# Kernel optimization log

Hardware: AMD Instinct MI355X
Metric: run time of the kernel (lower is better)

## Reference

```python
import jax, jax.numpy as jnp
import numpy as np

B, N, D_IN = 32, 4096, 768
D_SLOT, K = 256, 8
D_SHAPE, D_TEX = 128, 128
NUM_ITERS = 3
EPS = 1e-8
LN_EPS = 1e-5


def _ln(x, g, b):
    m = jnp.mean(x, axis=-1, keepdims=True)
    v = jnp.mean((x - m) ** 2, axis=-1, keepdims=True)
    return (x - m) * jax.lax.rsqrt(v + LN_EPS) * g + b


def setup_inputs() -> dict:
    key = jax.random.key(0)
    ks = jax.random.split(key, 20)
    s = lambda fan_in: 1.0 / np.sqrt(fan_in)
    d = {}
    d['features'] = jax.random.normal(ks[0], (B, N, D_IN), dtype=jnp.float32)
    # slot init MLP: d_input -> 2*d_slot -> K*d_slot
    d['Wi1'] = jax.random.uniform(ks[1], (D_IN, 2 * D_SLOT), minval=-s(D_IN), maxval=s(D_IN))
    d['bi1'] = jnp.zeros((2 * D_SLOT,), jnp.float32)
    d['Wi2'] = jax.random.uniform(ks[2], (2 * D_SLOT, K * D_SLOT), minval=-s(2 * D_SLOT), maxval=s(2 * D_SLOT))
    d['bi2'] = jnp.zeros((K * D_SLOT,), jnp.float32)
    # input_proj Linear + LayerNorm
    d['Wp'] = jax.random.uniform(ks[3], (D_IN, D_SLOT), minval=-s(D_IN), maxval=s(D_IN))
    d['bp'] = jnp.zeros((D_SLOT,), jnp.float32)
    d['ln_in_g'] = jnp.ones((D_SLOT,), jnp.float32)
    d['ln_in_b'] = jnp.zeros((D_SLOT,), jnp.float32)
    # attention projections (no bias)
    d['Wqs'] = jax.random.uniform(ks[4], (D_SHAPE, D_SHAPE), minval=-s(D_SHAPE), maxval=s(D_SHAPE))
    d['Wks'] = jax.random.uniform(ks[5], (D_SHAPE, D_SHAPE), minval=-s(D_SHAPE), maxval=s(D_SHAPE))
    d['Wqt'] = jax.random.uniform(ks[6], (D_TEX, D_TEX), minval=-s(D_TEX), maxval=s(D_TEX))
    d['Wkt'] = jax.random.uniform(ks[7], (D_TEX, D_TEX), minval=-s(D_TEX), maxval=s(D_TEX))
    # GRUCell (PyTorch layout, gate order r,z,n), stored as [in, 3*hidden]
    d['W_ih'] = jax.random.uniform(ks[8], (D_SLOT, 3 * D_SLOT), minval=-s(D_SLOT), maxval=s(D_SLOT))
    d['W_hh'] = jax.random.uniform(ks[9], (D_SLOT, 3 * D_SLOT), minval=-s(D_SLOT), maxval=s(D_SLOT))
    d['b_ih'] = jax.random.uniform(ks[10], (3 * D_SLOT,), minval=-s(D_SLOT), maxval=s(D_SLOT))
    d['b_hh'] = jax.random.uniform(ks[11], (3 * D_SLOT,), minval=-s(D_SLOT), maxval=s(D_SLOT))
    # slot LayerNorm + MLP
    d['ln_g'] = jnp.ones((D_SLOT,), jnp.float32)
    d['ln_b'] = jnp.zeros((D_SLOT,), jnp.float32)
    d['Wm1'] = jax.random.uniform(ks[12], (D_SLOT, 2 * D_SLOT), minval=-s(D_SLOT), maxval=s(D_SLOT))
    d['bm1'] = jnp.zeros((2 * D_SLOT,), jnp.float32)
    d['Wm2'] = jax.random.uniform(ks[13], (2 * D_SLOT, D_SLOT), minval=-s(2 * D_SLOT), maxval=s(2 * D_SLOT))
    d['bm2'] = jnp.zeros((D_SLOT,), jnp.float32)
    return d


def _gru(x, h, W_ih, W_hh, b_ih, b_hh):
    gx = x @ W_ih + b_ih  # [M, 3H]
    gh = h @ W_hh + b_hh
    xr, xz, xn = jnp.split(gx, 3, axis=-1)
    hr, hz, hn = jnp.split(gh, 3, axis=-1)
    r = jax.nn.sigmoid(xr + hr)
    z = jax.nn.sigmoid(xz + hz)
    n = jnp.tanh(xn + r * hn)
    return (1.0 - z) * n + z * h


def reference(features, Wi1, bi1, Wi2, bi2, Wp, bp, ln_in_g, ln_in_b,
              Wqs, Wks, Wqt, Wkt, W_ih, W_hh, b_ih, b_hh,
              ln_g, ln_b, Wm1, bm1, Wm2, bm2):
    gelu = lambda x: jax.nn.gelu(x, approximate=False)
    Bsz = features.shape[0]
    # input projection + LN: [B, N, D_SLOT]
    inputs = _ln(features @ Wp + bp, ln_in_g, ln_in_b)
    # probabilistic slot init (eval mode: deterministic branch only)
    feat_pool = jnp.mean(features, axis=1)  # [B, D_IN]
    slots = (gelu(feat_pool @ Wi1 + bi1) @ Wi2 + bi2).reshape(Bsz, K, D_SLOT)
    inp_s = inputs[:, :, :D_SHAPE]
    inp_t = inputs[:, :, D_SHAPE:]
    k_s = inp_s @ Wks  # [B, N, Ds]
    k_t = inp_t @ Wkt
    scale_s = D_SHAPE ** -0.5
    scale_t = D_TEX ** -0.5
    attn = None
    for _ in range(NUM_ITERS):
        q_s = slots[:, :, :D_SHAPE] @ Wqs  # [B, K, Ds]
        q_t = slots[:, :, D_SHAPE:] @ Wqt
        attn_shape = jnp.einsum('bkd,bnd->bkn', q_s, k_s) * scale_s
        attn_tex = jnp.einsum('bkd,bnd->bkn', q_t, k_t) * scale_t
        logits = 0.7 * attn_shape + 0.3 * attn_tex  # [B, K, N]
        attn = jax.nn.softmax(logits, axis=1)  # softmax over slots
        attn_normed = attn / (jnp.sum(attn, axis=-1, keepdims=True) + EPS)
        updates = jnp.einsum('bkn,bnd->bkd', attn_normed, inputs)
        h = _gru(updates.reshape(Bsz * K, D_SLOT), slots.reshape(Bsz * K, D_SLOT),
                 W_ih, W_hh, b_ih, b_hh).reshape(Bsz, K, D_SLOT)
        sn = _ln(h, ln_g, ln_b)
        slots = h + (gelu(sn @ Wm1 + bm1) @ Wm2 + bm2)
    return slots, attn, slots[:, :, :D_SHAPE], slots[:, :, D_SHAPE:]
```

## Files before the change

kernel.cpp:

```cpp
#include <hip/hip_runtime.h>
#include <math.h>

#define NB 32
#define NN 4096
#define DIN 768
#define DS 256
#define KS 8
#define MROWS (NB*NN)

typedef short s8v __attribute__((ext_vector_type(8)));
typedef float f4v __attribute__((ext_vector_type(4)));

__device__ __forceinline__ short f2bf(float f) {
    unsigned u = __builtin_bit_cast(unsigned, f);
    u = (u + 0x7FFFu + ((u >> 16) & 1u)) >> 16;
    return (short)u;
}
__device__ __forceinline__ float bf2f(short s) {
    unsigned u = ((unsigned)(unsigned short)s) << 16;
    return __builtin_bit_cast(float, u);
}
__device__ __forceinline__ float gelu_exact(float x) {
    return 0.5f * x * (1.0f + erff(x * 0.70710678118654752f));
}

__global__ __launch_bounds__(256) void prep_weights(const float* Wp, const float* Wks,
                                                    const float* Wkt, short* Wp_sw, short* Wk_sw) {
    int t = blockIdx.x * 256 + threadIdx.x;
    if (t < 24 * 16 * 64) {
        int s = t / (16 * 64), nt = (t / 64) % 16, l = t % 64;
        int q = l >> 4, m = l & 15;
        #pragma unroll
        for (int j = 0; j < 8; ++j)
            Wp_sw[t * 8 + j] = f2bf(Wp[(s * 32 + q * 8 + j) * 256 + nt * 16 + m]);
    } else if (t < 24 * 16 * 64 + 2 * 4 * 8 * 64) {
        int t2 = t - 24 * 16 * 64;
        int half = t2 / (4 * 8 * 64);
        int r = t2 % (4 * 8 * 64);
        int s = r / (8 * 64), nt = (r / 64) % 8, l = r % 64;
        int q = l >> 4, m = l & 15;
        const float* W = half ? Wkt : Wks;
        #pragma unroll
        for (int j = 0; j < 8; ++j)
            Wk_sw[t2 * 8 + j] = f2bf(W[(s * 32 + q * 8 + j) * 128 + nt * 16 + m]);
    }
}

__global__ __launch_bounds__(256, 2) void gemm_in_ln(const float* feat, const short* Wp_sw,
                                                     const float* bp, const float* g,
                                                     const float* bb, short* inputs_bf,
                                                     float* ppart) {
    __shared__ short Als[128 * 40];
    __shared__ short Bls[16 * 64 * 8];
    __shared__ float pool_ls[4][768];
    int tid = threadIdx.x;
    int wave = tid >> 6, lane = tid & 63, q = lane >> 4, m = lane & 15;
    long rowblk = (long)blockIdx.x * 128;
    f4v acc[2][16];
    #pragma unroll
    for (int rg = 0; rg < 2; ++rg)
        #pragma unroll
        for (int i = 0; i < 16; ++i) acc[rg][i] = (f4v){0, 0, 0, 0};
    for (int i = tid; i < 4 * 768; i += 256) (&pool_ls[0][0])[i] = 0.0f;
    __syncthreads();
    for (int s = 0; s < 24; ++s) {
        float4 v[4];
        #pragma unroll
        for (int p = 0; p < 4; ++p) {
            int idx = p * 256 + tid;
            int r = idx >> 3, cj = (idx & 7) * 4;
            v[p] = *(const float4*)(feat + (rowblk + r) * 768 + s * 32 + cj);
            short4 pk = make_short4(f2bf(v[p].x), f2bf(v[p].y), f2bf(v[p].z), f2bf(v[p].w));
            *(short4*)&Als[r * 40 + cj] = pk;
        }
        #pragma unroll
        for (int i = 0; i < 4; ++i) {
            int wb = i * 256 + wave * 64;
            __builtin_amdgcn_global_load_lds(
                (const __attribute__((address_space(1))) void*)(Wp_sw + (size_t)s * 8192 +
                                                               (size_t)(wb + lane) * 8),
                (__attribute__((address_space(3))) void*)&Bls[wb * 8], 16, 0, 0);
        }
        __syncthreads();
        {
            float px = v[0].x + v[1].x + v[2].x + v[3].x;
            float py = v[0].y + v[1].y + v[2].y + v[3].y;
            float pz = v[0].z + v[1].z + v[2].z + v[3].z;
            float pw = v[0].w + v[1].w + v[2].w + v[3].w;
            #pragma unroll
            for (int off = 8; off <= 32; off <<= 1) {
                px += __shfl_xor(px, off, 64);
                py += __shfl_xor(py, off, 64);
                pz += __shfl_xor(pz, off, 64);
                pw += __shfl_xor(pw, off, 64);
            }
            if (lane < 8) {
                int col = s * 32 + lane * 4;
                pool_ls[wave][col] += px;
                pool_ls[wave][col + 1] += py;
                pool_ls[wave][col + 2] += pz;
                pool_ls[wave][col + 3] += pw;
            }
        }
        s8v a0 = *(const s8v*)&Als[(wave * 32 + m) * 40 + q * 8];
        s8v a1 = *(const s8v*)&Als[(wave * 32 + 16 + m) * 40 + q * 8];
        #pragma unroll
        for (int nt = 0; nt < 16; ++nt) {
            s8v bf = *(const s8v*)&Bls[(nt * 64 + lane) * 8];
            acc[0][nt] = __builtin_amdgcn_mfma_f32_16x16x32_bf16(a0, bf, acc[0][nt], 0, 0, 0);
            acc[1][nt] = __builtin_amdgcn_mfma_f32_16x16x32_bf16(a1, bf, acc[1][nt], 0, 0, 0);
        }
        __syncthreads();
    }
    #pragma unroll
    for (int rg = 0; rg < 2; ++rg) {
        #pragma unroll
        for (int nt = 0; nt < 16; ++nt) {
            float bpv = bp[nt * 16 + m];
            #pragma unroll
            for (int r = 0; r < 4; ++r) acc[rg][nt][r] += bpv;
        }
        #pragma unroll
        for (int r = 0; r < 4; ++r) {
            float sm = 0, sq = 0;
            #pragma unroll
            for (int nt = 0; nt < 16; ++nt) { float vv = acc[rg][nt][r]; sm += vv; sq += vv * vv; }
            #pragma unroll
            for (int off = 1; off < 16; off <<= 1) {
                sm += __shfl_xor(sm, off, 16);
                sq += __shfl_xor(sq, off, 16);
            }
            float mean = sm * (1.0f / 256.0f);
            float var = sq * (1.0f / 256.0f) - mean * mean;
            float rstd = rsqrtf(var + 1e-5f);
            long grow = rowblk + wave * 32 + rg * 16 + q * 4 + r;
            #pragma unroll
            for (int nt = 0; nt < 16; ++nt) {
                int col = nt * 16 + m;
                float y = (acc[rg][nt][r] - mean) * rstd * g[col] + bb[col];
                inputs_bf[grow * 256 + col] = f2bf(y);
            }
        }
    }
    for (int d = tid; d < 768; d += 256) {
        ppart[(size_t)blockIdx.x * 768 + d] =
            pool_ls[0][d] + pool_ls[1][d] + pool_ls[2][d] + pool_ls[3][d];
    }
}

__global__ __launch_bounds__(256) void slots_hid(const float* ppart, const float* Wi1,
                                                 const float* bi1, float* hidb) {
    __shared__ float pool[768];
    int b = blockIdx.x, half = blockIdx.y, t = threadIdx.x;
    for (int i = 0; i < 3; ++i) {
        int d = t + i * 256;
        float s = 0;
        for (int c = 0; c < 32; ++c) s += ppart[(size_t)(b * 32 + c) * 768 + d];
        pool[d] = s * (1.0f / 4096.0f);
    }
    __syncthreads();
    int c = half * 256 + t;
    float acc = bi1[c];
    for (int j = 0; j < 768; ++j) acc += pool[j] * Wi1[j * 512 + c];
    hidb[b * 512 + c] = gelu_exact(acc);
}

__global__ __launch_bounds__(256) void slots_out(const float* hidb, const float* Wi2,
                                                 const float* bi2, float* slots) {
    __shared__ float hid[512];
    int b = blockIdx.x >> 3, sl = blockIdx.x & 7, t = threadIdx.x;
    hid[t] = hidb[b * 512 + t];
    hid[256 + t] = hidb[b * 512 + 256 + t];
    __syncthreads();
    int c = sl * 256 + t;
    float acc = bi2[c];
    for (int j = 0; j < 512; ++j) acc += hid[j] * Wi2[j * 2048 + c];
    slots[b * 2048 + c] = acc;
}

__global__ __launch_bounds__(256) void k_gemm(const short* inputs_bf, const short* Wk_sw,
                                              short* ksb, short* ktb) {
    int tid = threadIdx.x;
    int wave = tid >> 6, lane = tid & 63, q = lane >> 4, m = lane & 15;
    long rowblk = (long)blockIdx.x * 64;
    long arow = rowblk + wave * 16 + m;
    #pragma unroll
    for (int half = 0; half < 2; ++half) {
        f4v acc[8];
        #pragma unroll
        for (int i = 0; i < 8; ++i) acc[i] = (f4v){0, 0, 0, 0};
        const short* wkh = Wk_sw + half * 16384;
        #pragma unroll
        for (int s4 = 0; s4 < 4; ++s4) {
            s8v a = *(const s8v*)(inputs_bf + arow * 256 + half * 128 + s4 * 32 + q * 8);
            #pragma unroll
            for (int nt = 0; nt < 8; ++nt) {
                s8v bf = *(const s8v*)(wkh + ((s4 * 8 + nt) * 64 + lane) * 8);
                acc[nt] = __builtin_amdgcn_mfma_f32_16x16x32_bf16(a, bf, acc[nt], 0, 0, 0);
            }
        }
        short* out = half ? ktb : ksb;
        #pragma unroll
        for (int nt = 0; nt < 8; ++nt)
            #pragma unroll
            for (int r = 0; r < 4; ++r) {
                long grow = rowblk + wave * 16 + q * 4 + r;
                out[grow * 128 + nt * 16 + m] = f2bf(acc[nt][r]);
            }
    }
}

__global__ __launch_bounds__(256) void q_proj(const float* slots, const float* Wqs,
                                              const float* Wqt, float* qs, float* qt, float* S) {
    __shared__ float sl[1024];
    int b = blockIdx.x, half = blockIdx.y, t = threadIdx.x;
    if (half == 0 && t < 8) S[b * 8 + t] = 0.0f;
    for (int i = 0; i < 4; ++i) {
        int idx = i * 256 + t;
        int k = idx >> 7, d = idx & 127;
        sl[idx] = slots[(b * 8 + k) * 256 + half * 128 + d];
    }
    __syncthreads();
    const float* W = half ? Wqt : Wqs;
    float* out = half ? qt : qs;
    int d = t & 127;
    int k0 = (t >> 7) * 4;
    for (int k = k0; k < k0 + 4; ++k) {
        float acc = 0;
        for (int j = 0; j < 128; ++j) acc += sl[k * 128 + j] * W[j * 128 + d];
        out[(b * 8 + k) * 128 + d] = acc;
    }
}

__global__ __launch_bounds__(256) void attn_kernel(const short* ksb, const short* ktb,
                                                   const float* qs, const float* qt,
                                                   float* attn, float* S) {
    __shared__ float qls[1024], qlt[1024];
    __shared__ float red[32];
    int ntile = blockIdx.x, b = blockIdx.y, t = threadIdx.x;
    for (int i = 0; i < 4; ++i) {
        int idx = i * 256 + t;
        qls[idx] = qs[b * 1024 + idx];
        qlt[idx] = qt[b * 1024 + idx];
    }
    __syncthreads();
    long n0g = (long)b * 4096 + ntile * 512 + t;
    const short* krs0 = ksb + n0g * 128;
    const short* krt0 = ktb + n0g * 128;
    const short* krs1 = ksb + (n0g + 256) * 128;
    const short* krt1 = ktb + (n0g + 256) * 128;
    float accs0[8] = {0, 0, 0, 0, 0, 0, 0, 0};
    float acct0[8] = {0, 0, 0, 0, 0, 0, 0, 0};
    float accs1[8] = {0, 0, 0, 0, 0, 0, 0, 0};
    float acct1[8] = {0, 0, 0, 0, 0, 0, 0, 0};
    for (int c = 0; c < 16; ++c) {
        s8v vs0 = *(const s8v*)(krs0 + c * 8);
        s8v vt0 = *(const s8v*)(krt0 + c * 8);
        s8v vs1 = *(const s8v*)(krs1 + c * 8);
        s8v vt1 = *(const s8v*)(krt1 + c * 8);
        float fs0[8], ft0[8], fs1[8], ft1[8];
        #pragma unroll
        for (int j = 0; j < 8; ++j) {
            fs0[j] = bf2f(vs0[j]); ft0[j] = bf2f(vt0[j]);
            fs1[j] = bf2f(vs1[j]); ft1[j] = bf2f(vt1[j]);
        }
        #pragma unroll
        for (int k = 0; k < 8; ++k) {
            float as0 = 0, at0 = 0, as1 = 0, at1 = 0;
            #pragma unroll
            for (int j = 0; j < 8; ++j) {
                float qv_s = qls[k * 128 + c * 8 + j];
                float qv_t = qlt[k * 128 + c * 8 + j];
                as0 += qv_s * fs0[j]; as1 += qv_s * fs1[j];
                at0 += qv_t * ft0[j]; at1 += qv_t * ft1[j];
            }
            accs0[k] += as0; acct0[k] += at0;
            accs1[k] += as1; acct1[k] += at1;
        }
    }
    const float cs = 0.7f * 0.08838834764831845f;
    const float ct = 0.3f * 0.08838834764831845f;
    float lg0[8], lg1[8];
    float mx0 = -1e30f, mx1 = -1e30f;
    #pragma unroll
    for (int k = 0; k < 8; ++k) {
        lg0[k] = accs0[k] * cs + acct0[k] * ct; mx0 = fmaxf(mx0, lg0[k]);
        lg1[k] = accs1[k] * cs + acct1[k] * ct; mx1 = fmaxf(mx1, lg1[k]);
    }
    float se0 = 0, se1 = 0;
    #pragma unroll
    for (int k = 0; k < 8; ++k) {
        lg0[k] = expf(lg0[k] - mx0); se0 += lg0[k];
        lg1[k] = expf(lg1[k] - mx1); se1 += lg1[k];
    }
    float inv0 = 1.0f / se0, inv1 = 1.0f / se1;
    int nn0 = ntile * 512 + t;
    #pragma unroll
    for (int k = 0; k < 8; ++k) {
        float a0 = lg0[k] * inv0;
        float a1 = lg1[k] * inv1;
        attn[((long)(b * 8 + k)) * 4096 + nn0] = a0;
        attn[((long)(b * 8 + k)) * 4096 + nn0 + 256] = a1;
        lg0[k] = a0 + a1;
    }
    int lane = t & 63, wv = t >> 6;
    #pragma unroll
    for (int k = 0; k < 8; ++k) {
        float v = lg0[k];
        #pragma unroll
        for (int off = 1; off < 64; off <<= 1) v += __shfl_xor(v, off, 64);
        if (lane == 0) red[wv * 8 + k] = v;
    }
    __syncthreads();
    if (t < 8) {
        float s = red[t] + red[8 + t] + red[16 + t] + red[24 + t];
        atomicAdd(&S[b * 8 + t], s);
    }
}

__global__ __launch_bounds__(256) void updates_kernel(const short* inputs_bf, const float* attn,
                                                      const float* S, float* upart) {
    __shared__ unsigned inls[64 * 32];
    __shared__ float atls[8 * 64];
    int bid = blockIdx.x;
    int b = bid >> 4, dt = (bid >> 2) & 3, nq = bid & 3;
    int t = threadIdx.x;
    int k = t >> 5, dp = t & 31;
    float rk = 1.0f / (S[b * 8 + k] + 1e-8f);
    float a0 = 0, a1 = 0;
    for (int ch = 0; ch < 16; ++ch) {
        long n0 = nq * 1024 + ch * 64;
        #pragma unroll
        for (int p = 0; p < 2; ++p) {
            int idx = p * 256 + t;
            int rr = idx >> 3, cc = idx & 7;
            *(uint4*)&inls[rr * 32 + cc * 4] =
                *(const uint4*)(inputs_bf + ((long)b * 4096 + n0 + rr) * 256 + dt * 64 + cc * 8);
        }
        {
            int c2 = (t & 31) * 2;
            float2 av = *(const float2*)(attn + ((long)(b * 8 + k)) * 4096 + n0 + c2);
            atls[k * 64 + c2] = av.x * rk;
            atls[k * 64 + c2 + 1] = av.y * rk;
        }
        __syncthreads();
        #pragma unroll
        for (int j = 0; j < 64; ++j) {
            float a = atls[k * 64 + j];
            unsigned u = inls[j * 32 + dp];
            a0 += a * bf2f((short)(u & 0xFFFF));
            a1 += a * bf2f((short)(u >> 16));
        }
        __syncthreads();
    }
    int bk = b * 8 + k;
    upart[((nq * 256 + bk) * 256) + dt * 64 + dp * 2] = a0;
    upart[((nq * 256 + bk) * 256) + dt * 64 + dp * 2 + 1] = a1;
}

__global__ __launch_bounds__(256) void gru_kernel(const float* upart, const float* W_ih,
                                                  const float* W_hh, const float* b_ih,
                                                  const float* b_hh, const float* ln_g,
                                                  const float* ln_b, const float* Wm1,
                                                  const float* bm1, const float* Wm2,
                                                  const float* bm2, float* slots) {
    __shared__ float u[256], h[256], sn[256], hid[512];
    __shared__ float redA[4], redB[4];
    int bk = blockIdx.x, t = threadIdx.x;
    u[t] = upart[(0 * 256 + bk) * 256 + t] + upart[(1 * 256 + bk) * 256 + t] +
           upart[(2 * 256 + bk) * 256 + t] + upart[(3 * 256 + bk) * 256 + t];
    h[t] = slots[bk * 256 + t];
    __syncthreads();
    float xr = b_ih[t], xz = b_ih[256 + t], xn = b_ih[512 + t];
    float hr = b_hh[t], hz = b_hh[256 + t], hn = b_hh[512 + t];
    for (int j = 0; j < 256; ++j) {
        float uj = u[j], hj = h[j];
        const float* wi = W_ih + j * 768 + t;
        const float* wh = W_hh + j * 768 + t;
        xr += uj * wi[0]; xz += uj * wi[256]; xn += uj * wi[512];
        hr += hj * wh[0]; hz += hj * wh[256]; hn += hj * wh[512];
    }
    float rg = 1.0f / (1.0f + expf(-(xr + hr)));
    float zg = 1.0f / (1.0f + expf(-(xz + hz)));
    float ng = tanhf(xn + rg * hn);
    float hnew = (1.0f - zg) * ng + zg * h[t];
    float v1 = hnew, v2 = hnew * hnew;
    int lane = t & 63, wv = t >> 6;
    #pragma unroll
    for (int off = 1; off < 64; off <<= 1) {
        v1 += __shfl_xor(v1, off, 64);
        v2 += __shfl_xor(v2, off, 64);
    }
    if (lane == 0) { redA[wv] = v1; redB[wv] = v2; }
    __syncthreads();
    float sm = redA[0] + redA[1] + redA[2] + redA[3];
    float sq = redB[0] + redB[1] + redB[2] + redB[3];
    float mean = sm * (1.0f / 256.0f);
    float var = sq * (1.0f / 256.0f) - mean * mean;
    float rstd = rsqrtf(var + 1e-5f);
    sn[t] = (hnew - mean) * rstd * ln_g[t] + ln_b[t];
    __syncthreads();
    float m1 = bm1[t], m2 = bm1[256 + t];
    for (int j = 0; j < 256; ++j) {
        float s = sn[j];
        m1 += s * Wm1[j * 512 + t];
        m2 += s * Wm1[j * 512 + 256 + t];
    }
    hid[t] = gelu_exact(m1);
    hid[256 + t] = gelu_exact(m2);
    __syncthreads();
    float o = bm2[t];
    for (int j = 0; j < 512; ++j) o += hid[j] * Wm2[j * 256 + t];
    slots[bk * 256 + t] = hnew + o;
}

__global__ __launch_bounds__(256) void pack_out(const float* slots, const float* attn,
                                                float* out) {
    long i = (long)blockIdx.x * 256 + threadIdx.x;
    if (i >= 1179648) return;
    float v;
    if (i < 65536) v = slots[i];
    else if (i < 1114112) v = attn[i - 65536];
    else {
        long j = i - 1114112;
        if (j < 32768) v = slots[(j >> 7) * 256 + (j & 127)];
        else { long j2 = j - 32768; v = slots[(j2 >> 7) * 256 + 128 + (j2 & 127)]; }
    }
    out[i] = v;
}

extern "C" void kernel_launch(void* const* d_in, const int* in_sizes, int n_in,
                              void* d_out, int out_size, void* d_ws, size_t ws_size,
                              hipStream_t stream) {
    const float* feat    = (const float*)d_in[0];
    const float* Wi1     = (const float*)d_in[1];
    const float* bi1     = (const float*)d_in[2];
    const float* Wi2     = (const float*)d_in[3];
    const float* bi2     = (const float*)d_in[4];
    const float* Wp      = (const float*)d_in[5];
    const float* bp      = (const float*)d_in[6];
    const float* ln_in_g = (const float*)d_in[7];
    const float* ln_in_b = (const float*)d_in[8];
    const float* Wqs     = (const float*)d_in[9];
    const float* Wks     = (const float*)d_in[10];
    const float* Wqt     = (const float*)d_in[11];
    const float* Wkt     = (const float*)d_in[12];
    const float* W_ih    = (const float*)d_in[13];
    const float* W_hh    = (const float*)d_in[14];
    const float* b_ih    = (const float*)d_in[15];
    const float* b_hh    = (const float*)d_in[16];
    const float* ln_g    = (const float*)d_in[17];
    const float* ln_b    = (const float*)d_in[18];
    const float* Wm1     = (const float*)d_in[19];
    const float* bm1     = (const float*)d_in[20];
    const float* Wm2     = (const float*)d_in[21];
    const float* bm2     = (const float*)d_in[22];
    float* out = (float*)d_out;

    char* ws = (char*)d_ws;
    short* inputs_bf = (short*)ws; ws += 67108864;
    short* ksb       = (short*)ws; ws += 33554432;
    short* ktb       = (short*)ws; ws += 33554432;
    float* attn      = (float*)ws; ws += 4194304;
    float* slots     = (float*)ws; ws += 262144;
    float* qsb       = (float*)ws; ws += 131072;
    float* qtb       = (float*)ws; ws += 131072;
    float* ppart     = (float*)ws; ws += 3145728;
    short* Wp_sw     = (short*)ws; ws += 393216;
    short* Wk_sw     = (short*)ws; ws += 65536;
    float* hidb      = (float*)ws; ws += 65536;
    float* S         = (float*)ws; ws += 1024;
    float* upart     = (float*)ws; ws += 1048576;

    prep_weights<<<112, 256, 0, stream>>>(Wp, Wks, Wkt, Wp_sw, Wk_sw);
    gemm_in_ln<<<1024, 256, 0, stream>>>(feat, Wp_sw, bp, ln_in_g, ln_in_b, inputs_bf, ppart);
    slots_hid<<<dim3(32, 2), 256, 0, stream>>>(ppart, Wi1, bi1, hidb);
    slots_out<<<256, 256, 0, stream>>>(hidb, Wi2, bi2, slots);
    k_gemm<<<2048, 256, 0, stream>>>(inputs_bf, Wk_sw, ksb, ktb);
    for (int it = 0; it < 3; ++it) {
        q_proj<<<dim3(32, 2), 256, 0, stream>>>(slots, Wqs, Wqt, qsb, qtb, S);
        attn_kernel<<<dim3(8, 32), 256, 0, stream>>>(ksb, ktb, qsb, qtb, attn, S);
        updates_kernel<<<512, 256, 0, stream>>>(inputs_bf, attn, S, upart);
        gru_kernel<<<256, 256, 0, stream>>>(upart, W_ih, W_hh, b_ih, b_hh, ln_g, ln_b,
                                            Wm1, bm1, Wm2, bm2, slots);
    }
    pack_out<<<4608, 256, 0, stream>>>(slots, attn, out);
}
```

Before: 1.101 ms.

## Fuse K projection into input GEMM, write attn directly to output, widen updates

The separate K-projection kernel is folded into the input projection + LayerNorm kernel. The normalized bf16 tile is staged in shared memory (in a union with the GEMM buffers), stored to global with coalesced writes, and reused for the Ks/Kt MFMA GEMMs, so inputs_bf no longer has to be re-read. Attention is written straight into the output buffer, so pack_out only copies slots. updates_kernel now handles 128 columns per block with half as many blocks. The costs are more LDS use and extra epilogue work in the fused kernel, which may reduce occupancy.

```diff
diff --git a/kernel.cpp b/kernel.cpp
--- a/kernel.cpp
+++ b/kernel.cpp
@@ -46,13 +46,18 @@
     }
 }
 
+struct SA {
+    short Als[128 * 40];
+    short Bls[16 * 64 * 8];
+    float pool[4][768];
+};
+
 __global__ __launch_bounds__(256, 2) void gemm_in_ln(const float* feat, const short* Wp_sw,
-                                                     const float* bp, const float* g,
-                                                     const float* bb, short* inputs_bf,
-                                                     float* ppart) {
-    __shared__ short Als[128 * 40];
-    __shared__ short Bls[16 * 64 * 8];
-    __shared__ float pool_ls[4][768];
+                                                     const short* Wk_sw, const float* bp,
+                                                     const float* g, const float* bb,
+                                                     short* inputs_bf, float* ppart,
+                                                     short* ksb, short* ktb) {
+    __shared__ union { SA a; short tile[128 * 264]; } sh;
     int tid = threadIdx.x;
     int wave = tid >> 6, lane = tid & 63, q = lane >> 4, m = lane & 15;
     long rowblk = (long)blockIdx.x * 128;
@@ -61,7 +66,7 @@
     for (int rg = 0; rg < 2; ++rg)
         #pragma unroll
         for (int i = 0; i < 16; ++i) acc[rg][i] = (f4v){0, 0, 0, 0};
-    for (int i = tid; i < 4 * 768; i += 256) (&pool_ls[0][0])[i] = 0.0f;
+    for (int i = tid; i < 4 * 768; i += 256) (&sh.a.pool[0][0])[i] = 0.0f;
     __syncthreads();
     for (int s = 0; s < 24; ++s) {
         float4 v[4];
@@ -71,7 +76,7 @@
             int r = idx >> 3, cj = (idx & 7) * 4;
             v[p] = *(const float4*)(feat + (rowblk + r) * 768 + s * 32 + cj);
             short4 pk = make_short4(f2bf(v[p].x), f2bf(v[p].y), f2bf(v[p].z), f2bf(v[p].w));
-            *(short4*)&Als[r * 40 + cj] = pk;
+            *(short4*)&sh.a.Als[r * 40 + cj] = pk;
         }
         #pragma unroll
         for (int i = 0; i < 4; ++i) {
@@ -79,7 +84,7 @@
             __builtin_amdgcn_global_load_lds(
                 (const __attribute__((address_space(1))) void*)(Wp_sw + (size_t)s * 8192 +
                                                                (size_t)(wb + lane) * 8),
-                (__attribute__((address_space(3))) void*)&Bls[wb * 8], 16, 0, 0);
+                (__attribute__((address_space(3))) void*)&sh.a.Bls[wb * 8], 16, 0, 0);
         }
         __syncthreads();
         {
@@ -96,22 +101,27 @@
             }
             if (lane < 8) {
                 int col = s * 32 + lane * 4;
-                pool_ls[wave][col] += px;
-                pool_ls[wave][col + 1] += py;
-                pool_ls[wave][col + 2] += pz;
-                pool_ls[wave][col + 3] += pw;
+                sh.a.pool[wave][col] += px;
+                sh.a.pool[wave][col + 1] += py;
+                sh.a.pool[wave][col + 2] += pz;
+                sh.a.pool[wave][col + 3] += pw;
             }
         }
-        s8v a0 = *(const s8v*)&Als[(wave * 32 + m) * 40 + q * 8];
-        s8v a1 = *(const s8v*)&Als[(wave * 32 + 16 + m) * 40 + q * 8];
+        s8v a0 = *(const s8v*)&sh.a.Als[(wave * 32 + m) * 40 + q * 8];
+        s8v a1 = *(const s8v*)&sh.a.Als[(wave * 32 + 16 + m) * 40 + q * 8];
         #pragma unroll
         for (int nt = 0; nt < 16; ++nt) {
-            s8v bf = *(const s8v*)&Bls[(nt * 64 + lane) * 8];
+            s8v bf = *(const s8v*)&sh.a.Bls[(nt * 64 + lane) * 8];
             acc[0][nt] = __builtin_amdgcn_mfma_f32_16x16x32_bf16(a0, bf, acc[0][nt], 0, 0, 0);
             acc[1][nt] = __builtin_amdgcn_mfma_f32_16x16x32_bf16(a1, bf, acc[1][nt], 0, 0, 0);
         }
         __syncthreads();
     }
+    for (int d = tid; d < 768; d += 256) {
+        ppart[(size_t)blockIdx.x * 768 + d] =
+            sh.a.pool[0][d] + sh.a.pool[1][d] + sh.a.pool[2][d] + sh.a.pool[3][d];
+    }
+    __syncthreads();
     #pragma unroll
     for (int rg = 0; rg < 2; ++rg) {
         #pragma unroll
@@ -133,18 +143,53 @@
             float mean = sm * (1.0f / 256.0f);
             float var = sq * (1.0f / 256.0f) - mean * mean;
             float rstd = rsqrtf(var + 1e-5f);
-            long grow = rowblk + wave * 32 + rg * 16 + q * 4 + r;
+            int lr = wave * 32 + rg * 16 + q * 4 + r;
             #pragma unroll
             for (int nt = 0; nt < 16; ++nt) {
                 int col = nt * 16 + m;
                 float y = (acc[rg][nt][r] - mean) * rstd * g[col] + bb[col];
-                inputs_bf[grow * 256 + col] = f2bf(y);
+                sh.tile[lr * 264 + col] = f2bf(y);
             }
         }
     }
-    for (int d = tid; d < 768; d += 256) {
-        ppart[(size_t)blockIdx.x * 768 + d] =
-            pool_ls[0][d] + pool_ls[1][d] + pool_ls[2][d] + pool_ls[3][d];
+    __syncthreads();
+    #pragma unroll
+    for (int p = 0; p < 16; ++p) {
+        int idx = p * 256 + tid;
+        int rr = idx >> 5, cc = idx & 31;
+        uint4 w = *(const uint4*)&sh.tile[rr * 264 + cc * 8];
+        *(uint4*)(inputs_bf + (rowblk + rr) * 256 + cc * 8) = w;
+    }
+    int rb = wave * 32;
+    #pragma unroll
+    for (int half = 0; half < 2; ++half) {
+        f4v kacc[2][8];
+        #pragma unroll
+        for (int rg = 0; rg < 2; ++rg)
+            #pragma unroll
+            for (int i = 0; i < 8; ++i) kacc[rg][i] = (f4v){0, 0, 0, 0};
+        const short* wkh = Wk_sw + half * 16384;
+        #pragma unroll
+        for (int s4 = 0; s4 < 4; ++s4) {
+            s8v a0 = *(const s8v*)&sh.tile[(rb + m) * 264 + half * 128 + s4 * 32 + q * 8];
+            s8v a1 = *(const s8v*)&sh.tile[(rb + 16 + m) * 264 + half * 128 + s4 * 32 + q * 8];
+            #pragma unroll
+            for (int nt = 0; nt < 8; ++nt) {
+                s8v bf = *(const s8v*)(wkh + ((s4 * 8 + nt) * 64 + lane) * 8);
+                kacc[0][nt] = __builtin_amdgcn_mfma_f32_16x16x32_bf16(a0, bf, kacc[0][nt], 0, 0, 0);
+                kacc[1][nt] = __builtin_amdgcn_mfma_f32_16x16x32_bf16(a1, bf, kacc[1][nt], 0, 0, 0);
+            }
+        }
+        short* outk = half ? ktb : ksb;
+        #pragma unroll
+        for (int rg = 0; rg < 2; ++rg)
+            #pragma unroll
+            for (int nt = 0; nt < 8; ++nt)
+                #pragma unroll
+                for (int r = 0; r < 4; ++r) {
+                    long grow = rowblk + rb + rg * 16 + q * 4 + r;
+                    outk[grow * 128 + nt * 16 + m] = f2bf(kacc[rg][nt][r]);
+                }
     }
 }
 
@@ -176,38 +221,6 @@
     float acc = bi2[c];
     for (int j = 0; j < 512; ++j) acc += hid[j] * Wi2[j * 2048 + c];
     slots[b * 2048 + c] = acc;
-}
-
-__global__ __launch_bounds__(256) void k_gemm(const short* inputs_bf, const short* Wk_sw,
-                                              short* ksb, short* ktb) {
-    int tid = threadIdx.x;
-    int wave = tid >> 6, lane = tid & 63, q = lane >> 4, m = lane & 15;
-    long rowblk = (long)blockIdx.x * 64;
-    long arow = rowblk + wave * 16 + m;
-    #pragma unroll
-    for (int half = 0; half < 2; ++half) {
-        f4v acc[8];
-        #pragma unroll
-        for (int i = 0; i < 8; ++i) acc[i] = (f4v){0, 0, 0, 0};
-        const short* wkh = Wk_sw + half * 16384;
-        #pragma unroll
-        for (int s4 = 0; s4 < 4; ++s4) {
-            s8v a = *(const s8v*)(inputs_bf + arow * 256 + half * 128 + s4 * 32 + q * 8);
-            #pragma unroll
-            for (int nt = 0; nt < 8; ++nt) {
-                s8v bf = *(const s8v*)(wkh + ((s4 * 8 + nt) * 64 + lane) * 8);
-                acc[nt] = __builtin_amdgcn_mfma_f32_16x16x32_bf16(a, bf, acc[nt], 0, 0, 0);
-            }
-        }
-        short* out = half ? ktb : ksb;
-        #pragma unroll
-        for (int nt = 0; nt < 8; ++nt)
-            #pragma unroll
-            for (int r = 0; r < 4; ++r) {
-                long grow = rowblk + wave * 16 + q * 4 + r;
-                out[grow * 128 + nt * 16 + m] = f2bf(acc[nt][r]);
-            }
-    }
 }
 
 __global__ __launch_bounds__(256) void q_proj(const float* slots, const float* Wqs,
@@ -320,42 +333,44 @@
 
 __global__ __launch_bounds__(256) void updates_kernel(const short* inputs_bf, const float* attn,
                                                       const float* S, float* upart) {
-    __shared__ unsigned inls[64 * 32];
+    __shared__ unsigned inls[64 * 64];
     __shared__ float atls[8 * 64];
     int bid = blockIdx.x;
-    int b = bid >> 4, dt = (bid >> 2) & 3, nq = bid & 3;
+    int b = bid >> 3, dth = (bid >> 2) & 1, nq = bid & 3;
     int t = threadIdx.x;
     int k = t >> 5, dp = t & 31;
     float rk = 1.0f / (S[b * 8 + k] + 1e-8f);
-    float a0 = 0, a1 = 0;
+    float a0 = 0, a1 = 0, a2 = 0, a3 = 0;
     for (int ch = 0; ch < 16; ++ch) {
-        long n0 = nq * 1024 + ch * 64;
-        #pragma unroll
-        for (int p = 0; p < 2; ++p) {
+        long n0 = (long)nq * 1024 + ch * 64;
+        #pragma unroll
+        for (int p = 0; p < 4; ++p) {
             int idx = p * 256 + t;
-            int rr = idx >> 3, cc = idx & 7;
-            *(uint4*)&inls[rr * 32 + cc * 4] =
-                *(const uint4*)(inputs_bf + ((long)b * 4096 + n0 + rr) * 256 + dt * 64 + cc * 8);
+            int rr = idx >> 4, cc = idx & 15;
+            *(uint4*)&inls[rr * 64 + cc * 4] =
+                *(const uint4*)(inputs_bf + ((long)b * 4096 + n0 + rr) * 256 + dth * 128 + cc * 8);
         }
         {
-            int c2 = (t & 31) * 2;
+            int c2 = dp * 2;
             float2 av = *(const float2*)(attn + ((long)(b * 8 + k)) * 4096 + n0 + c2);
             atls[k * 64 + c2] = av.x * rk;
             atls[k * 64 + c2 + 1] = av.y * rk;
         }
         __syncthreads();
-        #pragma unroll
+        #pragma unroll 16
         for (int j = 0; j < 64; ++j) {
             float a = atls[k * 64 + j];
-            unsigned u = inls[j * 32 + dp];
-            a0 += a * bf2f((short)(u & 0xFFFF));
-            a1 += a * bf2f((short)(u >> 16));
+            uint2 uu = *(const uint2*)&inls[j * 64 + dp * 2];
+            a0 += a * bf2f((short)(uu.x & 0xFFFF));
+            a1 += a * bf2f((short)(uu.x >> 16));
+            a2 += a * bf2f((short)(uu.y & 0xFFFF));
+            a3 += a * bf2f((short)(uu.y >> 16));
         }
         __syncthreads();
     }
     int bk = b * 8 + k;
-    upart[((nq * 256 + bk) * 256) + dt * 64 + dp * 2] = a0;
-    upart[((nq * 256 + bk) * 256) + dt * 64 + dp * 2 + 1] = a1;
+    float* o = upart + ((long)(nq * 256 + bk)) * 256 + dth * 128 + dp * 4;
+    o[0] = a0; o[1] = a1; o[2] = a2; o[3] = a3;
 }
 
 __global__ __launch_bounds__(256) void gru_kernel(const float* upart, const float* W_ih,
@@ -414,19 +429,18 @@
     slots[bk * 256 + t] = hnew + o;
 }
 
-__global__ __launch_bounds__(256) void pack_out(const float* slots, const float* attn,
-                                                float* out) {
-    long i = (long)blockIdx.x * 256 + threadIdx.x;
-    if (i >= 1179648) return;
+__global__ __launch_bounds__(256) void pack_out(const float* slots, float* out) {
+    int i = blockIdx.x * 256 + threadIdx.x;
     float v;
-    if (i < 65536) v = slots[i];
-    else if (i < 1114112) v = attn[i - 65536];
+    long o;
+    if (i < 65536) { o = i; v = slots[i]; }
     else {
-        long j = i - 1114112;
+        int j = i - 65536;
+        o = 1114112 + (long)j;
         if (j < 32768) v = slots[(j >> 7) * 256 + (j & 127)];
-        else { long j2 = j - 32768; v = slots[(j2 >> 7) * 256 + 128 + (j2 & 127)]; }
-    }
-    out[i] = v;
+        else { int j2 = j - 32768; v = slots[(j2 >> 7) * 256 + 128 + (j2 & 127)]; }
+    }
+    out[o] = v;
 }
 
 extern "C" void kernel_launch(void* const* d_in, const int* in_sizes, int n_in,
@@ -456,12 +470,13 @@
     const float* Wm2     = (const float*)d_in[21];
     const float* bm2     = (const float*)d_in[22];
     float* out = (float*)d_out;
+    float* outAttn = out + 65536;
 
     char* ws = (char*)d_ws;
     short* inputs_bf = (short*)ws; ws += 67108864;
     short* ksb       = (short*)ws; ws += 33554432;
     short* ktb       = (short*)ws; ws += 33554432;
-    float* attn      = (float*)ws; ws += 4194304;
+    ws += 4194304;
     float* slots     = (float*)ws; ws += 262144;
     float* qsb       = (float*)ws; ws += 131072;
     float* qtb       = (float*)ws; ws += 131072;
@@ -473,16 +488,16 @@
     float* upart     = (float*)ws; ws += 1048576;
 
     prep_weights<<<112, 256, 0, stream>>>(Wp, Wks, Wkt, Wp_sw, Wk_sw);
-    gemm_in_ln<<<1024, 256, 0, stream>>>(feat, Wp_sw, bp, ln_in_g, ln_in_b, inputs_bf, ppart);
+    gemm_in_ln<<<1024, 256, 0, stream>>>(feat, Wp_sw, Wk_sw, bp, ln_in_g, ln_in_b,
+                                         inputs_bf, ppart, ksb, ktb);
     slots_hid<<<dim3(32, 2), 256, 0, stream>>>(ppart, Wi1, bi1, hidb);
     slots_out<<<256, 256, 0, stream>>>(hidb, Wi2, bi2, slots);
-    k_gemm<<<2048, 256, 0, stream>>>(inputs_bf, Wk_sw, ksb, ktb);
     for (int it = 0; it < 3; ++it) {
         q_proj<<<dim3(32, 2), 256, 0, stream>>>(slots, Wqs, Wqt, qsb, qtb, S);
-        attn_kernel<<<dim3(8, 32), 256, 0, stream>>>(ksb, ktb, qsb, qtb, attn, S);
-        updates_kernel<<<512, 256, 0, stream>>>(inputs_bf, attn, S, upart);
+        attn_kernel<<<dim3(8, 32), 256, 0, stream>>>(ksb, ktb, qsb, qtb, outAttn, S);
+        updates_kernel<<<256, 256, 0, stream>>>(inputs_bf, outAttn, S, upart);
         gru_kernel<<<256, 256, 0, stream>>>(upart, W_ih, W_hh, b_ih, b_hh, ln_g, ln_b,
                                             Wm1, bm1, Wm2, bm2, slots);
     }
-    pack_out<<<4608, 256, 0, stream>>>(slots, attn, out);
-}
+    pack_out<<<512, 256, 0, stream>>>(slots, out);
+}
```

Measured after the change: 1.169 ms. 1.06x slower.

## Fuse q-projection and output packing into GRU kernel, drop atomics

Applied to the files above, without the earlier changes.

The per-iteration q_proj launch is folded into the tail of the GRU kernel, so each block projects its new slot row into qs/qt. Attention is written directly into the output buffer, and the final GRU iteration writes the slot outputs, which removes the pack_out kernel and its copy of the attention map. Per-tile row sums go to a partial-sum array that updates_kernel reduces, replacing the atomicAdd and the zeroing of S. This trades a few launches and about 4 MB of copying for slightly more work per GRU block.

```diff
diff --git a/kernel.cpp b/kernel.cpp
--- a/kernel.cpp
+++ b/kernel.cpp
@@ -211,10 +211,9 @@
 }
 
 __global__ __launch_bounds__(256) void q_proj(const float* slots, const float* Wqs,
-                                              const float* Wqt, float* qs, float* qt, float* S) {
+                                              const float* Wqt, float* qs, float* qt) {
     __shared__ float sl[1024];
     int b = blockIdx.x, half = blockIdx.y, t = threadIdx.x;
-    if (half == 0 && t < 8) S[b * 8 + t] = 0.0f;
     for (int i = 0; i < 4; ++i) {
         int idx = i * 256 + t;
         int k = idx >> 7, d = idx & 127;
@@ -234,7 +233,7 @@
 
 __global__ __launch_bounds__(256) void attn_kernel(const short* ksb, const short* ktb,
                                                    const float* qs, const float* qt,
-                                                   float* attn, float* S) {
+                                                   float* attn, float* Spart) {
     __shared__ float qls[1024], qlt[1024];
     __shared__ float red[32];
     int ntile = blockIdx.x, b = blockIdx.y, t = threadIdx.x;
@@ -314,19 +313,22 @@
     __syncthreads();
     if (t < 8) {
         float s = red[t] + red[8 + t] + red[16 + t] + red[24 + t];
-        atomicAdd(&S[b * 8 + t], s);
+        Spart[(b * 8 + t) * 8 + ntile] = s;
     }
 }
 
 __global__ __launch_bounds__(256) void updates_kernel(const short* inputs_bf, const float* attn,
-                                                      const float* S, float* upart) {
+                                                      const float* Spart, float* upart) {
     __shared__ unsigned inls[64 * 32];
     __shared__ float atls[8 * 64];
     int bid = blockIdx.x;
     int b = bid >> 4, dt = (bid >> 2) & 3, nq = bid & 3;
     int t = threadIdx.x;
     int k = t >> 5, dp = t & 31;
-    float rk = 1.0f / (S[b * 8 + k] + 1e-8f);
+    const float* spp = Spart + (b * 8 + k) * 8;
+    float sp = ((spp[0] + spp[1]) + (spp[2] + spp[3])) +
+               ((spp[4] + spp[5]) + (spp[6] + spp[7]));
+    float rk = 1.0f / (sp + 1e-8f);
     float a0 = 0, a1 = 0;
     for (int ch = 0; ch < 16; ++ch) {
         long n0 = nq * 1024 + ch * 64;
@@ -363,7 +365,9 @@
                                                   const float* b_hh, const float* ln_g,
                                                   const float* ln_b, const float* Wm1,
                                                   const float* bm1, const float* Wm2,
-                                                  const float* bm2, float* slots) {
+                                                  const float* bm2, float* slots,
+                                                  const float* Wqs, const float* Wqt,
+                                                  float* qs, float* qt, float* out, int final_it) {
     __shared__ float u[256], h[256], sn[256], hid[512];
     __shared__ float redA[4], redB[4];
     int bk = blockIdx.x, t = threadIdx.x;
@@ -411,22 +415,21 @@
     __syncthreads();
     float o = bm2[t];
     for (int j = 0; j < 512; ++j) o += hid[j] * Wm2[j * 256 + t];
-    slots[bk * 256 + t] = hnew + o;
-}
-
-__global__ __launch_bounds__(256) void pack_out(const float* slots, const float* attn,
-                                                float* out) {
-    long i = (long)blockIdx.x * 256 + threadIdx.x;
-    if (i >= 1179648) return;
-    float v;
-    if (i < 65536) v = slots[i];
-    else if (i < 1114112) v = attn[i - 65536];
-    else {
-        long j = i - 1114112;
-        if (j < 32768) v = slots[(j >> 7) * 256 + (j & 127)];
-        else { long j2 = j - 32768; v = slots[(j2 >> 7) * 256 + 128 + (j2 & 127)]; }
-    }
-    out[i] = v;
+    float v = hnew + o;
+    slots[bk * 256 + t] = v;
+    if (!final_it) {
+        u[t] = v;
+        __syncthreads();
+        int half = t >> 7, d = t & 127;
+        const float* W = half ? Wqt : Wqs;
+        float qa = 0;
+        for (int j = 0; j < 128; ++j) qa += u[half * 128 + j] * W[j * 128 + d];
+        (half ? qt : qs)[bk * 128 + d] = qa;
+    } else {
+        out[bk * 256 + t] = v;
+        if (t < 128) out[1114112 + bk * 128 + t] = v;
+        else out[1114112 + 32768 + bk * 128 + (t - 128)] = v;
+    }
 }
 
 extern "C" void kernel_launch(void* const* d_in, const int* in_sizes, int n_in,
@@ -456,12 +459,13 @@
     const float* Wm2     = (const float*)d_in[21];
     const float* bm2     = (const float*)d_in[22];
     float* out = (float*)d_out;
+    float* outAttn = out + 65536;
 
     char* ws = (char*)d_ws;
     short* inputs_bf = (short*)ws; ws += 67108864;
     short* ksb       = (short*)ws; ws += 33554432;
     short* ktb       = (short*)ws; ws += 33554432;
-    float* attn      = (float*)ws; ws += 4194304;
+    ws += 4194304;
     float* slots     = (float*)ws; ws += 262144;
     float* qsb       = (float*)ws; ws += 131072;
     float* qtb       = (float*)ws; ws += 131072;
@@ -469,7 +473,7 @@
     short* Wp_sw     = (short*)ws; ws += 393216;
     short* Wk_sw     = (short*)ws; ws += 65536;
     float* hidb      = (float*)ws; ws += 65536;
-    float* S         = (float*)ws; ws += 1024;
+    float* Spart     = (float*)ws; ws += 8192;
     float* upart     = (float*)ws; ws += 1048576;
 
     prep_weights<<<112, 256, 0, stream>>>(Wp, Wks, Wkt, Wp_sw, Wk_sw);
@@ -477,12 +481,12 @@
     slots_hid<<<dim3(32, 2), 256, 0, stream>>>(ppart, Wi1, bi1, hidb);
     slots_out<<<256, 256, 0, stream>>>(hidb, Wi2, bi2, slots);
     k_gemm<<<2048, 256, 0, stream>>>(inputs_bf, Wk_sw, ksb, ktb);
+    q_proj<<<dim3(32, 2), 256, 0, stream>>>(slots, Wqs, Wqt, qsb, qtb);
     for (int it = 0; it < 3; ++it) {
-        q_proj<<<dim3(32, 2), 256, 0, stream>>>(slots, Wqs, Wqt, qsb, qtb, S);
-        attn_kernel<<<dim3(8, 32), 256, 0, stream>>>(ksb, ktb, qsb, qtb, attn, S);
-        updates_kernel<<<512, 256, 0, stream>>>(inputs_bf, attn, S, upart);
+        attn_kernel<<<dim3(8, 32), 256, 0, stream>>>(ksb, ktb, qsb, qtb, outAttn, Spart);
+        updates_kernel<<<512, 256, 0, stream>>>(inputs_bf, outAttn, Spart, upart);
         gru_kernel<<<256, 256, 0, stream>>>(upart, W_ih, W_hh, b_ih, b_hh, ln_g, ln_b,
-                                            Wm1, bm1, Wm2, bm2, slots);
-    }
-    pack_out<<<4608, 256, 0, stream>>>(slots, attn, out);
-}
+                                            Wm1, bm1, Wm2, bm2, slots,
+                                            Wqs, Wqt, qsb, qtb, out, it == 2 ? 1 : 0);
+    }
+}
```

Result: no change. 1.081 ms (-1.8%).
